# Performance work log

Hardware: AMD Instinct MI355X
Metric: run time of the kernel (lower is better)

## Reference

```python
import jax, jax.numpy as jnp
import numpy as np

P = 256  # patch_size (init kwarg)


def _unfold3s2(g):
    # g: [B,1,P,P] -> [B,9,L], kernel 3, stride 2, torch Unfold ordering (kh outer, kw inner)
    B = g.shape[0]
    n = (P - 3) // 2 + 1
    cols = [g[:, 0, di:di + 2 * n - 1:2, dj:dj + 2 * n - 1:2]
            for di in range(3) for dj in range(3)]  # each [B,n,n]
    return jnp.stack(cols, axis=1).reshape(B, 9, n * n)


def _fold3s2(patches):
    # patches: [..., 9, L] -> [..., P, P], overlap-add (torch Fold, kernel 3, stride 2)
    lead = patches.shape[:-2]
    n = (P - 3) // 2 + 1
    p = patches.reshape(*lead, 3, 3, n, n)
    out = jnp.zeros((*lead, P, P), patches.dtype)
    for di in range(3):
        for dj in range(3):
            out = out.at[..., di:di + 2 * n - 1:2, dj:dj + 2 * n - 1:2].add(p[..., di, dj, :, :])
    return out


def _maxpool3x3(x):
    # MaxPool2d(3, stride=1, padding=1) on NCHW
    return jax.lax.reduce_window(x, -jnp.inf, jax.lax.max,
                                 (1, 1, 3, 3), (1, 1, 1, 1),
                                 [(0, 0), (0, 0), (1, 1), (1, 1)])


def setup_inputs() -> dict:
    key = jax.random.key(0)
    k1, k2 = jax.random.split(key)
    x = jax.random.uniform(k1, (2, 3, P, P), dtype=jnp.float32)
    ref = jax.random.uniform(k2, (2, 3, P, P), dtype=jnp.float32)
    return {"x": x, "ref": ref, "k": 4}


def reference(x, ref, k):
    B = x.shape[0]
    L = ((P - 3) // 2 + 1) ** 2
    # grayscale proxies
    x_gray = jnp.max(_maxpool3x3(x), axis=1, keepdims=True) - jnp.min(x, axis=1, keepdims=True)
    ref_gray = jnp.mean(ref, axis=1, keepdims=True)
    input_patch = _unfold3s2(x_gray)   # [B,9,L]
    ref_patch = _unfold3s2(ref_gray)   # [B,9,L]
    # faithful to original: mean over patch index (dim 2), norm of UNCENTERED patches over dim 1
    input_norm = (input_patch - jnp.mean(input_patch, axis=2, keepdims=True)) \
        / jnp.linalg.norm(input_patch, axis=1, keepdims=True)
    ref_norm = (ref_patch - jnp.mean(ref_patch, axis=2, keepdims=True)) \
        / jnp.linalg.norm(ref_patch, axis=1, keepdims=True)
    ncc = jnp.einsum('bpl,bpm->blm', input_norm, ref_norm)  # [B,L,L]
    _, idx = jax.lax.top_k(ncc, k)                           # idx: [B,L,k]
    # gather best-matching ref patches for all k at once: [B,k,9,L]
    idx_t = jnp.transpose(idx, (0, 2, 1))                    # [B,k,L]
    ind = jnp.broadcast_to(idx_t[:, :, None, :], (B, k, 9, L))
    src = jnp.broadcast_to(ref_patch[:, None], (B, k, 9, L))
    gathered = jnp.take_along_axis(src, ind, axis=3)         # [B,k,9,L]
    folded = _fold3s2(gathered)                              # [B,k,P,P]
    return jnp.concatenate([x, folded], axis=1)              # [B,3+k,P,P]
```

## Files before the change

### kernel.cpp

```cpp
#include <hip/hip_runtime.h>
#include <math.h>
#include <float.h>

#define PSZ 256
#define NPATCH 127
#define L 16129
#define KTOP 4
#define TMAIN 256
#define RPT 2
#define ROWS_PER_BLOCK (TMAIN * RPT)
#define NROWBLK 32
#define NS 32
#define SEGLEN 505
#define MSTRIDE 508
#define ROWPAD 16384
#define GRP 8

typedef float f2 __attribute__((ext_vector_type(2)));

__device__ __forceinline__ f2 pk_fma(f2 a, f2 b, f2 c) {
  f2 d;
  asm("v_pk_fma_f32 %0, %1, %2, %3" : "=v"(d) : "v"(a), "v"(b), "v"(c));
  return d;
}
__device__ __forceinline__ f2 pk_mul(f2 a, f2 b) {
  f2 d;
  asm("v_pk_mul_f32 %0, %1, %2" : "=v"(d) : "v"(a), "v"(b));
  return d;
}

static constexpr size_t OFF_CMAX = 0;
static constexpr size_t OFF_CMIN = OFF_CMAX + 2 * PSZ * PSZ;
static constexpr size_t OFF_REFG = OFF_CMIN + 2 * PSZ * PSZ;
static constexpr size_t OFF_XG   = OFF_REFG + 2 * PSZ * PSZ;
static constexpr size_t OFF_MUI  = OFF_XG   + 2 * PSZ * PSZ;
static constexpr size_t OFF_MUR  = OFF_MUI  + 20;
static constexpr size_t OFF_A    = OFF_MUR  + 20;
static constexpr size_t OFF_B    = OFF_A    + 290324;
static constexpr size_t OFF_BT   = OFF_B    + 290324;
static constexpr size_t OFF_IDX  = OFF_BT   + 290324;
static constexpr size_t OFF_PV   = OFF_IDX  + 2 * L * 4;
static constexpr size_t OFF_PI   = OFF_PV   + (size_t)2 * NS * ROWPAD * 4;

__device__ __forceinline__ void insg(float rm, int gb,
    float& g0, float& g1, float& g2, float& g3,
    int& i0, int& i1, int& i2, int& i3) {
  bool c0 = rm > g0, c1 = rm > g1, c2 = rm > g2, c3 = rm > g3;
  g3 = c2 ? g2 : (c3 ? rm : g3);  i3 = c2 ? i2 : (c3 ? gb : i3);
  g2 = c1 ? g1 : (c2 ? rm : g2);  i2 = c1 ? i1 : (c2 ? gb : i2);
  g1 = c0 ? g0 : (c1 ? rm : g1);  i1 = c0 ? i0 : (c1 ? gb : i1);
  g0 = c0 ? rm : g0;              i0 = c0 ? gb : i0;
}

__device__ __forceinline__ void ins4c(float v, int m,
    float& v0, float& v1, float& v2, float& v3,
    int& x0, int& x1, int& x2, int& x3) {
  bool c0 = (v > v0) || (v == v0 && m < x0);
  bool c1 = (v > v1) || (v == v1 && m < x1);
  bool c2 = (v > v2) || (v == v2 && m < x2);
  bool c3 = (v > v3) || (v == v3 && m < x3);
  v3 = c2 ? v2 : (c3 ? v : v3);  x3 = c2 ? x2 : (c3 ? m : x3);
  v2 = c1 ? v1 : (c2 ? v : v2);  x2 = c1 ? x1 : (c2 ? m : x2);
  v1 = c0 ? v0 : (c1 ? v : v1);  x1 = c0 ? x0 : (c1 ? m : x1);
  v0 = c0 ? v : v0;              x0 = c0 ? m : x0;
}

__global__ void k1_pixel(const float* __restrict__ x, const float* __restrict__ ref,
                         float* __restrict__ ws, float* __restrict__ out) {
  int id = blockIdx.x * 256 + threadIdx.x;
  if (id >= 2 * PSZ * PSZ) return;
  int b = id >> 16;
  int pix = id & 0xFFFF;
  const float* xb = x + (size_t)b * 3 * PSZ * PSZ + pix;
  float c0 = xb[0], c1 = xb[PSZ * PSZ], c2 = xb[2 * PSZ * PSZ];
  ws[OFF_CMAX + id] = fmaxf(fmaxf(c0, c1), c2);
  ws[OFF_CMIN + id] = fminf(fminf(c0, c1), c2);
  const float* rb = ref + (size_t)b * 3 * PSZ * PSZ + pix;
  ws[OFF_REFG + id] = (rb[0] + rb[PSZ * PSZ] + rb[2 * PSZ * PSZ]) / 3.0f;
  float* ob = out + (size_t)b * 7 * PSZ * PSZ + pix;
  ob[0] = c0; ob[PSZ * PSZ] = c1; ob[2 * PSZ * PSZ] = c2;
}

__global__ void k2_gray(float* __restrict__ ws) {
  int id = blockIdx.x * 256 + threadIdx.x;
  if (id >= 2 * PSZ * PSZ) return;
  int b = id >> 16;
  int pix = id & 0xFFFF;
  int y = pix >> 8, xx = pix & 255;
  const float* cm = ws + OFF_CMAX + ((size_t)b << 16);
  float m = -3.402823466e+38f;
  for (int dy = -1; dy <= 1; ++dy) {
    int yy = y + dy;
    if (yy < 0 || yy > 255) continue;
    for (int dx = -1; dx <= 1; ++dx) {
      int xc = xx + dx;
      if (xc < 0 || xc > 255) continue;
      m = fmaxf(m, cm[yy * PSZ + xc]);
    }
  }
  ws[OFF_XG + id] = m - ws[OFF_CMIN + id];
}

__global__ void k4_mean(float* __restrict__ ws) {
  __shared__ double sm[1024];
  int which = blockIdx.x / 18;
  int bp = blockIdx.x % 18;
  int b = bp / 9, p = bp % 9;
  int di = p / 3, dj = p % 3;
  const float* g = ws + (which ? OFF_REFG : OFF_XG) + ((size_t)b << 16);
  int t = threadIdx.x;
  double s = 0.0;
  int l0 = t * 16;
  if (l0 < L) {
    int l1 = l0 + 16 < L ? l0 + 16 : L;
    int i = l0 / NPATCH, j = l0 % NPATCH;
    for (int l = l0; l < l1; ++l) {
      s += (double)g[(2 * i + di) * PSZ + 2 * j + dj];
      if (++j == NPATCH) { j = 0; ++i; }
    }
  }
  sm[t] = s;
  __syncthreads();
  for (int st = 512; st > 0; st >>= 1) {
    if (t < st) sm[t] += sm[t + st];
    __syncthreads();
  }
  if (t == 0)
    ws[(which ? OFF_MUR : OFF_MUI) + bp] = (float)(sm[0] / (double)L);
}

__global__ void k5_norm(float* __restrict__ ws) {
  int id = blockIdx.x * 256 + threadIdx.x;
  if (id >= 2 * L) return;
  int b = id / L, l = id % L;
  int i = l / NPATCH, j = l % NPATCH;
  const float* xg = ws + OFF_XG + ((size_t)b << 16);
  const float* rg = ws + OFF_REFG + ((size_t)b << 16);
  float vi[9], vr[9];
  float si = 0.f, sr = 0.f;
#pragma unroll
  for (int p = 0; p < 9; ++p) {
    int di = p / 3, dj = p % 3;
    vi[p] = xg[(2 * i + di) * PSZ + 2 * j + dj];
    vr[p] = rg[(2 * i + di) * PSZ + 2 * j + dj];
    si += vi[p] * vi[p];
    sr += vr[p] * vr[p];
  }
  float ni = sqrtf(si), nr = sqrtf(sr);
#pragma unroll
  for (int p = 0; p < 9; ++p) {
    float mi = ws[OFF_MUI + b * 9 + p];
    float mr = ws[OFF_MUR + b * 9 + p];
    float bn = (vr[p] - mr) / nr;
    ws[OFF_A + ((size_t)b * L + l) * 9 + p] = (vi[p] - mi) / ni;
    ws[OFF_B + ((size_t)b * 9 + p) * L + l] = bn;
    ws[OFF_BT + ((size_t)b * L + l) * 9 + p] = bn;
  }
}

__global__ __launch_bounds__(TMAIN, 1) void k6_topk(float* __restrict__ ws) {
  __shared__ float lds[9 * MSTRIDE];

  int bid = blockIdx.x;
  int seg = bid % NS;
  int rowblk = (bid / NS) % NROWBLK;
  int b = bid / (NS * NROWBLK);
  int m0 = seg * SEGLEN;
  int mend = m0 + SEGLEN;
  if (mend > L) mend = L;
  int mlen = mend - m0;

  const float* Bg = ws + OFF_B + (size_t)b * 9 * L + m0;
  for (int p = 0; p < 9; ++p)
    for (int mm = threadIdx.x; mm < mlen; mm += TMAIN)
      lds[p * MSTRIDE + mm] = Bg[(size_t)p * L + mm];
  __syncthreads();

  int row0 = rowblk * ROWS_PER_BLOCK + threadIdx.x * RPT;
  int r0 = row0 < L - 1 ? row0 : L - 1;
  int r1 = row0 + 1 < L - 1 ? row0 + 1 : L - 1;
  f2 va[9], vb[9];
  {
    const float* Ap0 = ws + OFF_A + ((size_t)b * L + r0) * 9;
    const float* Ap1 = ws + OFF_A + ((size_t)b * L + r1) * 9;
#pragma unroll
    for (int p = 0; p < 9; ++p) {
      float a0 = Ap0[p], a1 = Ap1[p];
      va[p].x = a0; va[p].y = a0;
      vb[p].x = a1; vb[p].y = a1;
    }
  }

  float g00 = -FLT_MAX, g01 = g00, g02 = g00, g03 = g00;
  float g10 = g00, g11 = g00, g12 = g00, g13 = g00;
  int i00 = 0, i01 = 0, i02 = 0, i03 = 0;
  int i10 = 0, i11 = 0, i12 = 0, i13 = 0;

  int ngrp = mlen >> 3;
  for (int g = 0; g < ngrp; ++g) {
    int mm = g << 3;
    f2 s0a, s0b, s0c, s0d, s1a, s1b, s1c, s1d;
#pragma unroll
    for (int p = 0; p < 9; ++p) {
      const float4* bp4 = reinterpret_cast<const float4*>(&lds[p * MSTRIDE + mm]);
      float4 q0 = bp4[0], q1 = bp4[1];
      f2 b0 = {q0.x, q0.y}, b1 = {q0.z, q0.w};
      f2 b2 = {q1.x, q1.y}, b3 = {q1.z, q1.w};
      if (p == 0) {
        s0a = pk_mul(va[0], b0); s0b = pk_mul(va[0], b1);
        s0c = pk_mul(va[0], b2); s0d = pk_mul(va[0], b3);
        s1a = pk_mul(vb[0], b0); s1b = pk_mul(vb[0], b1);
        s1c = pk_mul(vb[0], b2); s1d = pk_mul(vb[0], b3);
      } else {
        s0a = pk_fma(va[p], b0, s0a); s0b = pk_fma(va[p], b1, s0b);
        s0c = pk_fma(va[p], b2, s0c); s0d = pk_fma(va[p], b3, s0d);
        s1a = pk_fma(vb[p], b0, s1a); s1b = pk_fma(vb[p], b1, s1b);
        s1c = pk_fma(vb[p], b2, s1c); s1d = pk_fma(vb[p], b3, s1d);
      }
    }
    float rm0 = fmaxf(fmaxf(fmaxf(s0a.x, s0a.y), fmaxf(s0b.x, s0b.y)),
                      fmaxf(fmaxf(s0c.x, s0c.y), fmaxf(s0d.x, s0d.y)));
    float rm1 = fmaxf(fmaxf(fmaxf(s1a.x, s1a.y), fmaxf(s1b.x, s1b.y)),
                      fmaxf(fmaxf(s1c.x, s1c.y), fmaxf(s1d.x, s1d.y)));
    int gb = m0 + mm;
    insg(rm0, gb, g00, g01, g02, g03, i00, i01, i02, i03);
    insg(rm1, gb, g10, g11, g12, g13, i10, i11, i12, i13);
  }
  int tb = ngrp << 3;
  if (tb < mlen) {
    float rt0 = -FLT_MAX, rt1 = -FLT_MAX;
    for (int mm = tb; mm < mlen; ++mm) {
      float bb = lds[mm];
      float sv0 = va[0].x * bb, sv1 = vb[0].x * bb;
#pragma unroll
      for (int p = 1; p < 9; ++p) {
        bb = lds[p * MSTRIDE + mm];
        sv0 = fmaf(va[p].x, bb, sv0); sv1 = fmaf(vb[p].x, bb, sv1);
      }
      rt0 = fmaxf(rt0, sv0); rt1 = fmaxf(rt1, sv1);
    }
    insg(rt0, m0 + tb, g00, g01, g02, g03, i00, i01, i02, i03);
    insg(rt1, m0 + tb, g10, g11, g12, g13, i10, i11, i12, i13);
  }

  int* wsi = (int*)ws;
  if (row0 < L) {
    size_t base = (((size_t)b * NS + seg) * ROWPAD + row0) * 4;
    ws[OFF_PV + base + 0] = g00; ws[OFF_PV + base + 1] = g01;
    ws[OFF_PV + base + 2] = g02; ws[OFF_PV + base + 3] = g03;
    wsi[OFF_PI + base + 0] = i00; wsi[OFF_PI + base + 1] = i01;
    wsi[OFF_PI + base + 2] = i02; wsi[OFF_PI + base + 3] = i03;
  }
  if (row0 + 1 < L) {
    size_t base = (((size_t)b * NS + seg) * ROWPAD + row0 + 1) * 4;
    ws[OFF_PV + base + 0] = g10; ws[OFF_PV + base + 1] = g11;
    ws[OFF_PV + base + 2] = g12; ws[OFF_PV + base + 3] = g13;
    wsi[OFF_PI + base + 0] = i10; wsi[OFF_PI + base + 1] = i11;
    wsi[OFF_PI + base + 2] = i12; wsi[OFF_PI + base + 3] = i13;
  }
}

__global__ void k7_merge(float* __restrict__ ws) {
  int id = blockIdx.x * 256 + threadIdx.x;
  if (id >= 2 * L) return;
  int b = id / L, row = id % L;
  const int* wsi_c = (const int*)ws;

  float v0 = -FLT_MAX, v1 = v0, v2 = v0, v3 = v0;
  int x0 = 0x7FFFFFFF, x1 = x0, x2 = x0, x3 = x0;
  for (int s = 0; s < NS; ++s) {
    size_t base = (((size_t)b * NS + s) * ROWPAD + row) * 4;
#pragma unroll
    for (int q = 0; q < 4; ++q) {
      float val = ws[OFF_PV + base + q];
      int gb = wsi_c[OFF_PI + base + q];
      ins4c(val, gb, v0, v1, v2, v3, x0, x1, x2, x3);
    }
  }

  float a[9];
  const float* Ap = ws + OFF_A + ((size_t)b * L + row) * 9;
#pragma unroll
  for (int p = 0; p < 9; ++p) a[p] = Ap[p];

  int gbs[4] = {x0, x1, x2, x3};
  float w0 = -FLT_MAX, w1 = w0, w2 = w0, w3 = w0;
  int y0 = 0x7FFFFFFF, y1 = y0, y2 = y0, y3 = y0;
#pragma unroll
  for (int slot = 0; slot < 4; ++slot) {
    int gb = gbs[slot];
    int ge = gb + GRP; if (ge > L) ge = L;
    for (int mm = gb; mm < ge; ++mm) {
      const float* bt = ws + OFF_BT + ((size_t)b * L + mm) * 9;
      float s = a[0] * bt[0];
#pragma unroll
      for (int p = 1; p < 9; ++p) s = fmaf(a[p], bt[p], s);
      ins4c(s, mm, w0, w1, w2, w3, y0, y1, y2, y3);
    }
  }
  int* wsi = (int*)ws;
  size_t ib = OFF_IDX + (size_t)id * 4;
  wsi[ib] = y0; wsi[ib + 1] = y1; wsi[ib + 2] = y2; wsi[ib + 3] = y3;
}

__global__ void k8_fold(const float* __restrict__ ws, float* __restrict__ out) {
  int id = blockIdx.x * 256 + threadIdx.x;
  if (id >= 2 * KTOP * PSZ * PSZ) return;
  int b = id / (KTOP * PSZ * PSZ);
  int rem = id % (KTOP * PSZ * PSZ);
  int kk = rem >> 16;
  int pix = rem & 0xFFFF;
  int y = pix >> 8, xx = pix & 255;
  const int* wsi = (const int*)ws;
  const float* rg = ws + OFF_REFG + ((size_t)b << 16);
  float acc = 0.f;
  for (int di = 0; di < 3; ++di) {
    int yy = y - di;
    if (yy < 0 || (yy & 1) || (yy >> 1) >= NPATCH) continue;
    int i = yy >> 1;
    for (int dj = 0; dj < 3; ++dj) {
      int xc = xx - dj;
      if (xc < 0 || (xc & 1) || (xc >> 1) >= NPATCH) continue;
      int j = xc >> 1;
      int l = i * NPATCH + j;
      int m = wsi[OFF_IDX + ((size_t)b * L + l) * 4 + kk];
      int mi = m / NPATCH, mj = m % NPATCH;
      acc += rg[(2 * mi + di) * PSZ + 2 * mj + dj];
    }
  }
  out[(((size_t)b * 7 + 3 + kk) * PSZ + y) * PSZ + xx] = acc;
}

extern "C" void kernel_launch(void* const* d_in, const int* in_sizes, int n_in,
                              void* d_out, int out_size, void* d_ws, size_t ws_size,
                              hipStream_t stream) {
  const float* x = (const float*)d_in[0];
  const float* ref = (const float*)d_in[1];
  float* ws = (float*)d_ws;
  float* out = (float*)d_out;

  k1_pixel<<<512, 256, 0, stream>>>(x, ref, ws, out);
  k2_gray<<<512, 256, 0, stream>>>(ws);
  k4_mean<<<36, 1024, 0, stream>>>(ws);
  k5_norm<<<(2 * L + 255) / 256, 256, 0, stream>>>(ws);
  k6_topk<<<2 * NROWBLK * NS, TMAIN, 0, stream>>>(ws);
  k7_merge<<<(2 * L + 255) / 256, 256, 0, stream>>>(ws);
  k8_fold<<<(2 * KTOP * PSZ * PSZ + 255) / 256, 256, 0, stream>>>(ws, out);
}
```

Before: 238.4 us.

## Fuse pixel and gray kernels, widen top-k groups to 16, drop packed FMA

Merges the per-pixel channel reduction and 3x3 maxpool kernels into one tiled kernel that stages the channel max in shared memory with a halo, removing an intermediate global buffer and a launch. The top-k scan now takes one candidate max per 16 columns instead of 8, which halves insertion work. It also replaces the inline-asm packed FMA with scalar FMAs and raises launch bounds to 2 blocks per CU. The merge kernel rescans 16 columns per candidate, clamped to segment boundaries. The new kernel launches only 128 blocks, and the scalar FMAs may issue more instructions than the packed ones did.

```diff
diff --git a/kernel.cpp b/kernel.cpp
--- a/kernel.cpp
+++ b/kernel.cpp
@@ -14,24 +14,9 @@
 #define SEGLEN 505
 #define MSTRIDE 508
 #define ROWPAD 16384
-#define GRP 8
-
-typedef float f2 __attribute__((ext_vector_type(2)));
-
-__device__ __forceinline__ f2 pk_fma(f2 a, f2 b, f2 c) {
-  f2 d;
-  asm("v_pk_fma_f32 %0, %1, %2, %3" : "=v"(d) : "v"(a), "v"(b), "v"(c));
-  return d;
-}
-__device__ __forceinline__ f2 pk_mul(f2 a, f2 b) {
-  f2 d;
-  asm("v_pk_mul_f32 %0, %1, %2" : "=v"(d) : "v"(a), "v"(b));
-  return d;
-}
-
-static constexpr size_t OFF_CMAX = 0;
-static constexpr size_t OFF_CMIN = OFF_CMAX + 2 * PSZ * PSZ;
-static constexpr size_t OFF_REFG = OFF_CMIN + 2 * PSZ * PSZ;
+#define GRP 16
+
+static constexpr size_t OFF_REFG = 0;
 static constexpr size_t OFF_XG   = OFF_REFG + 2 * PSZ * PSZ;
 static constexpr size_t OFF_MUI  = OFF_XG   + 2 * PSZ * PSZ;
 static constexpr size_t OFF_MUR  = OFF_MUI  + 20;
@@ -65,40 +50,43 @@
   v0 = c0 ? v : v0;              x0 = c0 ? m : x0;
 }
 
-__global__ void k1_pixel(const float* __restrict__ x, const float* __restrict__ ref,
+__global__ void k12_gray(const float* __restrict__ x, const float* __restrict__ ref,
                          float* __restrict__ ws, float* __restrict__ out) {
-  int id = blockIdx.x * 256 + threadIdx.x;
-  if (id >= 2 * PSZ * PSZ) return;
-  int b = id >> 16;
-  int pix = id & 0xFFFF;
-  const float* xb = x + (size_t)b * 3 * PSZ * PSZ + pix;
-  float c0 = xb[0], c1 = xb[PSZ * PSZ], c2 = xb[2 * PSZ * PSZ];
-  ws[OFF_CMAX + id] = fmaxf(fmaxf(c0, c1), c2);
-  ws[OFF_CMIN + id] = fminf(fminf(c0, c1), c2);
-  const float* rb = ref + (size_t)b * 3 * PSZ * PSZ + pix;
-  ws[OFF_REFG + id] = (rb[0] + rb[PSZ * PSZ] + rb[2 * PSZ * PSZ]) / 3.0f;
-  float* ob = out + (size_t)b * 7 * PSZ * PSZ + pix;
-  ob[0] = c0; ob[PSZ * PSZ] = c1; ob[2 * PSZ * PSZ] = c2;
-}
-
-__global__ void k2_gray(float* __restrict__ ws) {
-  int id = blockIdx.x * 256 + threadIdx.x;
-  if (id >= 2 * PSZ * PSZ) return;
-  int b = id >> 16;
-  int pix = id & 0xFFFF;
-  int y = pix >> 8, xx = pix & 255;
-  const float* cm = ws + OFF_CMAX + ((size_t)b << 16);
-  float m = -3.402823466e+38f;
-  for (int dy = -1; dy <= 1; ++dy) {
-    int yy = y + dy;
-    if (yy < 0 || yy > 255) continue;
-    for (int dx = -1; dx <= 1; ++dx) {
-      int xc = xx + dx;
-      if (xc < 0 || xc > 255) continue;
-      m = fmaxf(m, cm[yy * PSZ + xc]);
-    }
-  }
-  ws[OFF_XG + id] = m - ws[OFF_CMIN + id];
+  __shared__ float sm[34][35];
+  int tile = blockIdx.x & 63;
+  int b = blockIdx.x >> 6;
+  int ty0 = (tile >> 3) << 5, tx0 = (tile & 7) << 5;
+  const float* xb = x + (size_t)b * 3 * 65536;
+  const float* rb = ref + (size_t)b * 3 * 65536;
+  for (int hid = threadIdx.x; hid < 34 * 34; hid += 256) {
+    int hy = hid / 34, hx = hid % 34;
+    int gy = ty0 + hy - 1, gx = tx0 + hx - 1;
+    float m = -FLT_MAX;
+    if (gy >= 0 && gy < 256 && gx >= 0 && gx < 256) {
+      int pix = gy * 256 + gx;
+      m = fmaxf(fmaxf(xb[pix], xb[65536 + pix]), xb[131072 + pix]);
+    }
+    sm[hy][hx] = m;
+  }
+  __syncthreads();
+  for (int iid = threadIdx.x; iid < 1024; iid += 256) {
+    int iy = iid >> 5, ix = iid & 31;
+    int gy = ty0 + iy, gx = tx0 + ix;
+    int pix = gy * 256 + gx;
+    float c0 = xb[pix], c1 = xb[65536 + pix], c2 = xb[131072 + pix];
+    float cmin = fminf(fminf(c0, c1), c2);
+    float mx = sm[iy][ix];
+#pragma unroll
+    for (int dy = 0; dy < 3; ++dy)
+#pragma unroll
+      for (int dx = 0; dx < 3; ++dx)
+        mx = fmaxf(mx, sm[iy + dy][ix + dx]);
+    size_t id = ((size_t)b << 16) + pix;
+    ws[OFF_XG + id] = mx - cmin;
+    ws[OFF_REFG + id] = (rb[pix] + rb[65536 + pix] + rb[131072 + pix]) / 3.0f;
+    float* ob = out + (size_t)b * 7 * 65536 + pix;
+    ob[0] = c0; ob[65536] = c1; ob[131072] = c2;
+  }
 }
 
 __global__ void k4_mean(float* __restrict__ ws) {
@@ -158,7 +146,7 @@
   }
 }
 
-__global__ __launch_bounds__(TMAIN, 1) void k6_topk(float* __restrict__ ws) {
+__global__ __launch_bounds__(TMAIN, 2) void k6_topk(float* __restrict__ ws) {
   __shared__ float lds[9 * MSTRIDE];
 
   int bid = blockIdx.x;
@@ -179,16 +167,12 @@
   int row0 = rowblk * ROWS_PER_BLOCK + threadIdx.x * RPT;
   int r0 = row0 < L - 1 ? row0 : L - 1;
   int r1 = row0 + 1 < L - 1 ? row0 + 1 : L - 1;
-  f2 va[9], vb[9];
+  float a0[9], a1[9];
   {
     const float* Ap0 = ws + OFF_A + ((size_t)b * L + r0) * 9;
     const float* Ap1 = ws + OFF_A + ((size_t)b * L + r1) * 9;
 #pragma unroll
-    for (int p = 0; p < 9; ++p) {
-      float a0 = Ap0[p], a1 = Ap1[p];
-      va[p].x = a0; va[p].y = a0;
-      vb[p].x = a1; vb[p].y = a1;
-    }
+    for (int p = 0; p < 9; ++p) { a0[p] = Ap0[p]; a1[p] = Ap1[p]; }
   }
 
   float g00 = -FLT_MAX, g01 = g00, g02 = g00, g03 = g00;
@@ -196,46 +180,43 @@
   int i00 = 0, i01 = 0, i02 = 0, i03 = 0;
   int i10 = 0, i11 = 0, i12 = 0, i13 = 0;
 
-  int ngrp = mlen >> 3;
-  for (int g = 0; g < ngrp; ++g) {
-    int mm = g << 3;
-    f2 s0a, s0b, s0c, s0d, s1a, s1b, s1c, s1d;
-#pragma unroll
-    for (int p = 0; p < 9; ++p) {
-      const float4* bp4 = reinterpret_cast<const float4*>(&lds[p * MSTRIDE + mm]);
-      float4 q0 = bp4[0], q1 = bp4[1];
-      f2 b0 = {q0.x, q0.y}, b1 = {q0.z, q0.w};
-      f2 b2 = {q1.x, q1.y}, b3 = {q1.z, q1.w};
-      if (p == 0) {
-        s0a = pk_mul(va[0], b0); s0b = pk_mul(va[0], b1);
-        s0c = pk_mul(va[0], b2); s0d = pk_mul(va[0], b3);
-        s1a = pk_mul(vb[0], b0); s1b = pk_mul(vb[0], b1);
-        s1c = pk_mul(vb[0], b2); s1d = pk_mul(vb[0], b3);
-      } else {
-        s0a = pk_fma(va[p], b0, s0a); s0b = pk_fma(va[p], b1, s0b);
-        s0c = pk_fma(va[p], b2, s0c); s0d = pk_fma(va[p], b3, s0d);
-        s1a = pk_fma(vb[p], b0, s1a); s1b = pk_fma(vb[p], b1, s1b);
-        s1c = pk_fma(vb[p], b2, s1c); s1d = pk_fma(vb[p], b3, s1d);
+  int nfull = mlen >> 4;
+  for (int g = 0; g < nfull; ++g) {
+    int mm = g << 4;
+    float rm0 = -FLT_MAX, rm1 = -FLT_MAX;
+#pragma unroll
+    for (int q = 0; q < 4; ++q) {
+      float s00, s01, s02, s03, s10, s11, s12, s13;
+#pragma unroll
+      for (int p = 0; p < 9; ++p) {
+        const float4 bq = *reinterpret_cast<const float4*>(&lds[p * MSTRIDE + mm + q * 4]);
+        if (p == 0) {
+          s00 = a0[0] * bq.x; s01 = a0[0] * bq.y; s02 = a0[0] * bq.z; s03 = a0[0] * bq.w;
+          s10 = a1[0] * bq.x; s11 = a1[0] * bq.y; s12 = a1[0] * bq.z; s13 = a1[0] * bq.w;
+        } else {
+          s00 = fmaf(a0[p], bq.x, s00); s01 = fmaf(a0[p], bq.y, s01);
+          s02 = fmaf(a0[p], bq.z, s02); s03 = fmaf(a0[p], bq.w, s03);
+          s10 = fmaf(a1[p], bq.x, s10); s11 = fmaf(a1[p], bq.y, s11);
+          s12 = fmaf(a1[p], bq.z, s12); s13 = fmaf(a1[p], bq.w, s13);
+        }
       }
-    }
-    float rm0 = fmaxf(fmaxf(fmaxf(s0a.x, s0a.y), fmaxf(s0b.x, s0b.y)),
-                      fmaxf(fmaxf(s0c.x, s0c.y), fmaxf(s0d.x, s0d.y)));
-    float rm1 = fmaxf(fmaxf(fmaxf(s1a.x, s1a.y), fmaxf(s1b.x, s1b.y)),
-                      fmaxf(fmaxf(s1c.x, s1c.y), fmaxf(s1d.x, s1d.y)));
+      rm0 = fmaxf(rm0, fmaxf(fmaxf(s00, s01), fmaxf(s02, s03)));
+      rm1 = fmaxf(rm1, fmaxf(fmaxf(s10, s11), fmaxf(s12, s13)));
+    }
     int gb = m0 + mm;
     insg(rm0, gb, g00, g01, g02, g03, i00, i01, i02, i03);
     insg(rm1, gb, g10, g11, g12, g13, i10, i11, i12, i13);
   }
-  int tb = ngrp << 3;
+  int tb = nfull << 4;
   if (tb < mlen) {
     float rt0 = -FLT_MAX, rt1 = -FLT_MAX;
     for (int mm = tb; mm < mlen; ++mm) {
       float bb = lds[mm];
-      float sv0 = va[0].x * bb, sv1 = vb[0].x * bb;
+      float sv0 = a0[0] * bb, sv1 = a1[0] * bb;
 #pragma unroll
       for (int p = 1; p < 9; ++p) {
         bb = lds[p * MSTRIDE + mm];
-        sv0 = fmaf(va[p].x, bb, sv0); sv1 = fmaf(vb[p].x, bb, sv1);
+        sv0 = fmaf(a0[p], bb, sv0); sv1 = fmaf(a1[p], bb, sv1);
       }
       rt0 = fmaxf(rt0, sv0); rt1 = fmaxf(rt1, sv1);
     }
@@ -289,7 +270,10 @@
 #pragma unroll
   for (int slot = 0; slot < 4; ++slot) {
     int gb = gbs[slot];
-    int ge = gb + GRP; if (ge > L) ge = L;
+    int se = (gb / SEGLEN + 1) * SEGLEN;
+    int ge = gb + GRP;
+    if (ge > se) ge = se;
+    if (ge > L) ge = L;
     for (int mm = gb; mm < ge; ++mm) {
       const float* bt = ws + OFF_BT + ((size_t)b * L + mm) * 9;
       float s = a[0] * bt[0];
@@ -339,8 +323,7 @@
   float* ws = (float*)d_ws;
   float* out = (float*)d_out;
 
-  k1_pixel<<<512, 256, 0, stream>>>(x, ref, ws, out);
-  k2_gray<<<512, 256, 0, stream>>>(ws);
+  k12_gray<<<128, 256, 0, stream>>>(x, ref, ws, out);
   k4_mean<<<36, 1024, 0, stream>>>(ws);
   k5_norm<<<(2 * L + 255) / 256, 256, 0, stream>>>(ws);
   k6_topk<<<2 * NROWBLK * NS, TMAIN, 0, stream>>>(ws);
```

After: 231.5 us. 2.9% less time.
